# Optimization experiments

Hardware: AMD Instinct MI355X
Metric: run time of the kernel (lower is better)

Reference implementation:

```python
import jax, jax.numpy as jnp
import numpy as np

B, T, LC = 64, 256, 16          # batch, seq_len, max word (char) length
WV, CV = 50000, 128             # word / char vocab
CE, WE = 100, 300               # char / word embedding dims
CH, WH = 100, 300               # char lstm hidden, word lstm hidden per direction
NT = 20                         # num tags
PAD, START, STOP = 0, 18, 19
NEG = -10000.0


def lstm(x, mask, W_ih, W_hh, b_ih, b_hh, reverse=False):
    """Masked LSTM (packed-sequence semantics). x:(N,L,D), mask:(N,L).
    Returns outputs (N,L,H) zeroed at padded steps and the final carried hidden (N,H)."""
    N = x.shape[0]
    H = W_hh.shape[1]
    h0 = jnp.zeros((N, H), x.dtype)
    c0 = jnp.zeros((N, H), x.dtype)

    def step(carry, inp):
        h, c = carry
        xt, mt = inp  # (N,D), (N,1)
        g = xt @ W_ih.T + h @ W_hh.T + (b_ih + b_hh)
        i, f, gg, o = jnp.split(g, 4, axis=-1)  # torch gate order i,f,g,o
        i = jax.nn.sigmoid(i); f = jax.nn.sigmoid(f)
        gg = jnp.tanh(gg); o = jax.nn.sigmoid(o)
        c_new = f * c + i * gg
        h_new = o * jnp.tanh(c_new)
        h = mt * h_new + (1.0 - mt) * h
        c = mt * c_new + (1.0 - mt) * c
        return (h, c), h * mt

    (hT, _), outs = jax.lax.scan(step, (h0, c0),
                                 (x.transpose(1, 0, 2), mask.T[:, :, None]),
                                 reverse=reverse)
    return outs.transpose(1, 0, 2), hT


def setup_inputs() -> dict:
    key = jax.random.key(0)
    ks = jax.random.split(key, 16)
    # trailing-padded word sequences (pack_padded semantics)
    lengths = jax.random.randint(ks[0], (B,), T // 4, T + 1)
    wmask = jnp.arange(T)[None, :] < lengths[:, None]
    word_x = jnp.where(wmask, jax.random.randint(ks[1], (B, T), 1, WV), 0)
    clens = jax.random.randint(ks[2], (B * T,), 1, LC + 1)
    cmask = (jnp.arange(LC)[None, :] < clens[:, None]) & wmask.reshape(-1)[:, None]
    char_x = jnp.where(cmask, jax.random.randint(ks[3], (B * T, LC), 1, CV), 0)
    y = jnp.where(wmask, jax.random.randint(ks[4], (B, T), 1, START), 0)

    def xav(k, shape):
        return jax.random.uniform(k, shape, jnp.float32, -1.0, 1.0) * jnp.sqrt(6.0 / (shape[0] + shape[1]))

    tr = jax.random.normal(ks[14], (NT, NT), jnp.float32)
    tr = tr.at[START, :].set(NEG).at[:, STOP].set(NEG)
    tr = tr.at[:, PAD].set(NEG).at[PAD, :].set(NEG)
    tr = tr.at[PAD, STOP].set(0.0).at[PAD, PAD].set(0.0)

    return dict(
        word_x=word_x, char_x=char_x, y=y,
        word_emb=jax.random.normal(ks[5], (WV, WE), jnp.float32) * 0.1,
        char_emb=jax.random.normal(ks[6], (CV, CE), jnp.float32) * 0.1,
        cW_ih=xav(ks[7], (4 * CH, CE)), cW_hh=xav(ks[8], (4 * CH, CH)),
        cb_ih=jnp.zeros(4 * CH), cb_hh=jnp.zeros(4 * CH),
        fW_ih=xav(ks[9], (4 * WH, WE + CH)), fW_hh=xav(ks[10], (4 * WH, WH)),
        fb_ih=jnp.zeros(4 * WH), fb_hh=jnp.zeros(4 * WH),
        bW_ih=xav(ks[11], (4 * WH, WE + CH)), bW_hh=xav(ks[12], (4 * WH, WH)),
        bb_ih=jnp.zeros(4 * WH), bb_hh=jnp.zeros(4 * WH),
        out_W=xav(ks[13], (NT, 2 * WH)), out_b=jnp.zeros(NT),
        transition=tr,
    )


def _forward(word_x, char_x, y, word_emb, char_emb,
             cW_ih, cW_hh, cb_ih, cb_hh,
             fW_ih, fW_hh, fb_ih, fb_hh,
             bW_ih, bW_hh, bb_ih, bb_hh,
             out_W, out_b, transition):
    mask = (word_x > 0).astype(jnp.float32)          # (B,T)
    cmask = (char_x > 0).astype(jnp.float32)         # (B*T,LC)
    # char LSTM: final carried hidden == output at last valid char; 0 for empty words
    _, c_h = lstm(char_emb[char_x], cmask, cW_ih, cW_hh, cb_ih, cb_hh)
    feat = jnp.concatenate([word_emb[word_x], c_h.reshape(B, T, CH)], axis=-1)  # (B,T,400)
    f_out, _ = lstm(feat, mask, fW_ih, fW_hh, fb_ih, fb_hh)
    b_out, _ = lstm(feat, mask, bW_ih, bW_hh, bb_ih, bb_hh, reverse=True)
    h = jnp.concatenate([f_out, b_out], axis=-1) @ out_W.T + out_b  # (B,T,NT)
    h = h * mask[:, :, None]

    # CRF log-partition (forward recurrence)
    def step(alpha, inp):
        ht, mt = inp  # (B,NT), (B,1)
        a_t = jax.nn.logsumexp(alpha[:, None, :] + transition[None, :, :] + ht[:, :, None], axis=-1)
        return mt * a_t + (1.0 - mt) * alpha, None

    alpha0 = jnp.full((B, NT), NEG, jnp.float32).at[:, START].set(0.0)
    alpha, _ = jax.lax.scan(step, alpha0, (h.transpose(1, 0, 2), mask.T[:, :, None]))
    Z = jax.nn.logsumexp(alpha + transition[STOP], axis=-1)  # (B,)

    # gold path score
    y_ext = jnp.concatenate([jnp.full((B, 1), START, y.dtype), y], axis=1)  # (B,T+1)
    emis = jnp.take_along_axis(h, y[:, :, None], axis=2)[..., 0]            # (B,T)
    tr_t = transition[y_ext[:, 1:], y_ext[:, :-1]]                          # (B,T)
    score = ((emis + tr_t) * mask).sum(axis=1)
    lengths = mask.sum(axis=1).astype(jnp.int32)
    last = jnp.take_along_axis(y_ext, lengths[:, None], axis=1)[:, 0]
    score = score + transition[STOP, last]
    return Z - score  # (B,) per-sequence NLL


def reference(word_x, char_x, y, word_emb, char_emb,
              cW_ih, cW_hh, cb_ih, cb_hh,
              fW_ih, fW_hh, fb_ih, fb_hh,
              bW_ih, bW_hh, bb_ih, bb_hh,
              out_W, out_b, transition):
    return _forward(word_x, char_x, y, word_emb, char_emb,
                    cW_ih, cW_hh, cb_ih, cb_hh,
                    fW_ih, fW_hh, fb_ih, fb_hh,
                    bW_ih, bW_hh, bb_ih, bb_hh,
                    out_W, out_b, transition)
```

## Files before the change

### kernel.cpp

```cpp
#include <hip/hip_runtime.h>

#define B_ 64
#define T_ 256
#define LC_ 16
#define CV_ 128
#define CE_ 100
#define WE_ 300
#define CH_ 100
#define WH_ 300
#define NTAG 20
#define START_ 18
#define STOP_ 19
#define NEG_ -10000.0f
#define NSEQ (B_*T_)
#define GW (4*WH_)
#define KF (WE_+CH_)
#define NW_ 25
#define UH_ 12
#define ROW_DW 164
#define SLOT_DW (64*ROW_DW)
#define HH_DW (2*257*SLOT_DW)
#define ZBLK ((HH_DW + 64 + 255)/256)

typedef unsigned short ushort_t;
typedef __attribute__((ext_vector_type(8))) short bf16x8;
typedef __attribute__((ext_vector_type(4))) float f32x4;
union BF8 { bf16x8 v; ushort_t u[8]; };

__device__ inline float bf2f(ushort_t u){ return __uint_as_float(((unsigned int)u)<<16); }
__device__ inline ushort_t f2bf(float f){
  unsigned int x = __float_as_uint(f);
  unsigned int r = (x + 0x7fffu + ((x>>16)&1u)) >> 16;
  return (ushort_t)r;
}
__device__ inline float sigm(float x){ return 1.f/(1.f+__expf(-x)); }
__device__ inline float ftanh(float x){
  float ax = fabsf(x);
  float e = __expf(-2.f*ax);
  float t = (1.f-e)/(1.f+e);
  return copysignf(t, x);
}
__device__ inline void gload_lds16(const unsigned* g, unsigned* l){
  __builtin_amdgcn_global_load_lds((const __attribute__((address_space(1))) unsigned*)g,
                                   (__attribute__((address_space(3))) unsigned*)l, 16, 0, 17);
}

__global__ __launch_bounds__(256) void k_prep(unsigned int* __restrict__ hh, int* __restrict__ flags,
    const float* __restrict__ cemb, const float* __restrict__ cWih,
    const float* __restrict__ cbih, const float* __restrict__ cbhh, float* __restrict__ Ec_t){
  int bid = blockIdx.x;
  if (bid < ZBLK){
    size_t idx = (size_t)bid*256 + threadIdx.x;
    if (idx < HH_DW) hh[idx] = 0u;
    else if (idx < HH_DW + 64) flags[idx - HH_DW] = 0;
  } else {
    int idx = (bid - ZBLK)*256 + threadIdx.x;
    int r = idx >> 7, c = idx & 127;
    float a = cbih[r] + cbhh[r];
    for (int k=0;k<CE_;++k) a += cemb[c*CE_+k]*cWih[r*CE_+k];
    Ec_t[c*400 + r] = a;
  }
}

__global__ __launch_bounds__(256) void k_char(const float* __restrict__ Ec_t,
    const float* __restrict__ Whh, const int* __restrict__ char_x,
    ushort_t* __restrict__ c_h){
  extern __shared__ char csm[];
  ushort_t* h_lds = (ushort_t*)csm;
  float*    g_lds = (float*)(csm + 64*132*2);
  const int tid  = threadIdx.x;
  const int lane = tid & 63;
  const int w    = tid >> 6;
  const int tb   = w*6;
  bf16x8 Bf[7][4];
  {
    int ntile = (w==3) ? 7 : 6;
    for (int tt=0; tt<ntile; ++tt){
      int r = (tb+tt)*16 + (lane & 15);
      #pragma unroll
      for (int ks=0; ks<4; ++ks){
        BF8 tmp;
        #pragma unroll
        for (int j=0; j<8; ++j){
          int k = 32*ks + 8*(lane>>4) + j;
          tmp.u[j] = (k < CH_) ? f2bf(Whh[(size_t)r*CH_ + k]) : (ushort_t)0;
        }
        Bf[tt][ks] = tmp.v;
      }
    }
  }
  for (int i=tid; i<64*132; i+=256) h_lds[i] = 0;
  const int seq_l = tid & 63;
  const int us    = tid >> 6;
  const int seqg  = blockIdx.x*64 + seq_l;
  const int u0    = us*25;
  float c_r[25], h_r[25];
  #pragma unroll
  for (int j=0;j<25;++j){ c_r[j]=0.f; h_r[j]=0.f; }
  const int* cx = char_x + (size_t)seqg*LC_;
  __syncthreads();
  #pragma unroll 1
  for (int t=0; t<LC_; ++t){
    #pragma unroll
    for (int m=0; m<4; ++m){
      int abase = (16*m + (lane&15))*132 + 8*(lane>>4);
      bf16x8 a0 = *(const bf16x8*)(h_lds + abase);
      bf16x8 a1 = *(const bf16x8*)(h_lds + abase + 32);
      bf16x8 a2 = *(const bf16x8*)(h_lds + abase + 64);
      bf16x8 a3 = *(const bf16x8*)(h_lds + abase + 96);
      int rw = 16*m + 4*(lane>>4);
      #pragma unroll
      for (int tt=0; tt<6; ++tt){
        f32x4 acc = {0,0,0,0};
        acc = __builtin_amdgcn_mfma_f32_16x16x32_bf16(a0, Bf[tt][0], acc, 0,0,0);
        acc = __builtin_amdgcn_mfma_f32_16x16x32_bf16(a1, Bf[tt][1], acc, 0,0,0);
        acc = __builtin_amdgcn_mfma_f32_16x16x32_bf16(a2, Bf[tt][2], acc, 0,0,0);
        acc = __builtin_amdgcn_mfma_f32_16x16x32_bf16(a3, Bf[tt][3], acc, 0,0,0);
        int col = (tb+tt)*16 + (lane&15);
        #pragma unroll
        for (int r4=0;r4<4;++r4) g_lds[(rw+r4)*401 + col] = acc[r4];
      }
      if (w == 3){
        f32x4 acc = {0,0,0,0};
        acc = __builtin_amdgcn_mfma_f32_16x16x32_bf16(a0, Bf[6][0], acc, 0,0,0);
        acc = __builtin_amdgcn_mfma_f32_16x16x32_bf16(a1, Bf[6][1], acc, 0,0,0);
        acc = __builtin_amdgcn_mfma_f32_16x16x32_bf16(a2, Bf[6][2], acc, 0,0,0);
        acc = __builtin_amdgcn_mfma_f32_16x16x32_bf16(a3, Bf[6][3], acc, 0,0,0);
        int col = 24*16 + (lane&15);
        #pragma unroll
        for (int r4=0;r4<4;++r4) g_lds[(rw+r4)*401 + col] = acc[r4];
      }
    }
    int ch = cx[t];
    __syncthreads();
    {
      const float* ec = Ec_t + (size_t)ch*400;
      const float* gr = g_lds + seq_l*401;
      #pragma unroll
      for (int j=0;j<25;++j){
        int u = u0 + j;
        float gi = gr[u        ] + ec[u        ];
        float gf = gr[100 + u  ] + ec[100 + u  ];
        float gg = gr[200 + u  ] + ec[200 + u  ];
        float go = gr[300 + u  ] + ec[300 + u  ];
        float I = sigm(gi), F = sigm(gf), G = ftanh(gg), O = sigm(go);
        float cn = F*c_r[j] + I*G;
        float hn = O*ftanh(cn);
        if (ch > 0){ c_r[j] = cn; h_r[j] = hn; }
        h_lds[seq_l*132 + u] = f2bf(h_r[j]);
      }
    }
    __syncthreads();
  }
  #pragma unroll
  for (int j=0;j<25;++j) c_h[(size_t)seqg*CH_ + u0 + j] = f2bf(h_r[j]);
}

__global__ __launch_bounds__(256) void k_feat(const int* __restrict__ word_x,
    const float* __restrict__ wemb, const ushort_t* __restrict__ c_h,
    ushort_t* __restrict__ feat){
  int gid = blockIdx.x*256 + threadIdx.x;
  int rf = gid / 100;
  int j4 = gid - rf*100;
  int k = 4*j4;
  int t = rf >> 6, b = rf & 63;
  int seq = b*T_ + t;
  ushort4 u;
  if (k < WE_){
    int wid = word_x[seq];
    float4 v = *(const float4*)&wemb[(size_t)wid*WE_ + k];
    u.x=f2bf(v.x); u.y=f2bf(v.y); u.z=f2bf(v.z); u.w=f2bf(v.w);
  } else {
    u = *(const ushort4*)&c_h[(size_t)seq*CH_ + (k - WE_)];
  }
  *(ushort4*)&feat[(size_t)rf*KF + k] = u;
}

__global__ __launch_bounds__(512, 2) void k_word2(
    const ushort_t* __restrict__ feat, unsigned int* __restrict__ hhd,
    const float* __restrict__ fWih, const float* __restrict__ fWhh,
    const float* __restrict__ fbih, const float* __restrict__ fbhh,
    const float* __restrict__ bWih, const float* __restrict__ bWhh,
    const float* __restrict__ bbih, const float* __restrict__ bbhh,
    const int* __restrict__ word_x, int* __restrict__ flags){
  extern __shared__ char smem[];
  ushort_t* h_s    = (ushort_t*)smem;
  ushort_t* f_s    = (ushort_t*)(smem + 64*328*2);
  float*    g_s    = (float*)   (smem + 64*328*2 + 64*416*2);
  unsigned* mask_s = (unsigned*)(smem + 64*328*2 + 64*416*2 + 64*52*4);
  const int tid  = threadIdx.x;
  const int lane = tid & 63;
  const int w    = tid >> 6;
  const int dir  = blockIdx.x & 1;
  const int g    = blockIdx.x >> 1;
  const int u0   = g * UH_;
  const int tm   = w & 3;
  const int grp  = w >> 2;
  const bool two = (grp == 0);
  const int tnb  = grp ? 2 : 0;
  const float* Wih = dir ? bWih : fWih;
  const float* Whh = dir ? bWhh : fWhh;
  const float* bi  = dir ? bbih : fbih;
  const float* bh  = dir ? bbhh : fbhh;
  int* myflags = flags + dir*32;

  bf16x8 B2[2][13], B1[2][10];
  {
    const int kb = 8*(lane >> 4);
    #pragma unroll
    for (int ti=0; ti<2; ++ti){
      if (ti == 0 || two){
        int nl = 16*(tnb+ti) + (lane & 15);
        int r  = (nl & 3)*WH_ + u0 + (nl >> 2);
        #pragma unroll
        for (int kk=0; kk<13; ++kk){
          BF8 tmp;
          #pragma unroll
          for (int j=0; j<8; ++j){
            int k = 32*kk + kb + j;
            tmp.u[j] = (k < KF) ? f2bf(Wih[(size_t)r*KF + k]) : (ushort_t)0;
          }
          B2[ti][kk] = tmp.v;
        }
        #pragma unroll
        for (int kk=0; kk<10; ++kk){
          BF8 tmp;
          #pragma unroll
          for (int j=0; j<8; ++j){
            int k = 32*kk + kb + j;
            tmp.u[j] = (k < WH_) ? f2bf(Whh[(size_t)r*WH_ + k]) : (ushort_t)0;
          }
          B1[ti][kk] = tmp.v;
        }
      }
    }
  }
  for (int idx=tid; idx<64*16; idx+=512){ f_s[(idx>>4)*416 + 400 + (idx & 15)] = 0; }
  if (tid < 512){
    int row = tid >> 3, dw = tid & 7;
    const int* wp = word_x + row*T_ + dw*32;
    unsigned bits = 0u;
    #pragma unroll
    for (int j4=0; j4<8; ++j4){
      int4 v = *(const int4*)(wp + 4*j4);
      bits |= (v.x>0 ? 1u:0u) << (4*j4);
      bits |= (v.y>0 ? 1u:0u) << (4*j4+1);
      bits |= (v.z>0 ? 1u:0u) << (4*j4+2);
      bits |= (v.w>0 ? 1u:0u) << (4*j4+3);
    }
    mask_s[row*8 + dw] = bits;
  }

  const int m_u = tid & 63;
  const int up  = tid >> 6;
  float4 bias_a = {0,0,0,0}, bias_b = {0,0,0,0};
  if (tid < 384){
    int u = u0 + 2*up;
    bias_a.x = bi[0*WH_+u] + bh[0*WH_+u];
    bias_a.y = bi[1*WH_+u] + bh[1*WH_+u];
    bias_a.z = bi[2*WH_+u] + bh[2*WH_+u];
    bias_a.w = bi[3*WH_+u] + bh[3*WH_+u];
    bias_b.x = bi[0*WH_+u+1] + bh[0*WH_+u+1];
    bias_b.y = bi[1*WH_+u+1] + bh[1*WH_+u+1];
    bias_b.z = bi[2*WH_+u+1] + bh[2*WH_+u+1];
    bias_b.w = bi[3*WH_+u+1] + bh[3*WH_+u+1];
  }
  float c_a=0.f, h_a=0.f, c_b=0.f, h_b=0.f;
  const int arow_f = (16*tm + (lane&15))*416 + 8*(lane>>4);
  const int arow_h = (16*tm + (lane&15))*328 + 8*(lane>>4);
  unsigned* h_sd = (unsigned*)h_s;
  __syncthreads();

  #pragma unroll 1
  for (int s=0; s<T_; ++s){
    int t = dir ? (T_-1-s) : s;
    {
      const ushort_t* fsrc = feat + (size_t)t*64*KF;
      for (int idx=tid; idx<3200; idx+=512){
        int m = idx/50, j = idx - m*50;
        uint4 v = *(const uint4*)(fsrc + m*KF + 8*j);
        *(uint4*)(f_s + m*416 + 8*j) = v;
      }
    }
    if (w == 0 && s > 0){
      bool act = lane < NW_;
      for (int it=0; it<2000000; ++it){
        int f = act ? __hip_atomic_load(myflags + lane, __ATOMIC_RELAXED, __HIP_MEMORY_SCOPE_AGENT)
                    : 0x7fffffff;
        if (__all(f >= s)) break;
        __builtin_amdgcn_s_sleep(1);
      }
    }
    __syncthreads();
    {
      const unsigned* hsrc = hhd + (size_t)(dir*257 + s)*SLOT_DW;
      #pragma unroll
      for (int i=0;i<6;++i){
        int idx = tid + 512*i;
        if (i < 5 || idx < 2624) gload_lds16(hsrc + 4*idx, h_sd + 4*idx);
      }
    }
    f32x4 acc0a = {0,0,0,0}, acc0b = {0,0,0,0}, acc1a = {0,0,0,0}, acc1b = {0,0,0,0};
    #pragma unroll
    for (int kk=0; kk<13; ++kk){
      bf16x8 a = *(const bf16x8*)(f_s + arow_f + 32*kk);
      if (kk & 1){
        acc0b = __builtin_amdgcn_mfma_f32_16x16x32_bf16(a, B2[0][kk], acc0b, 0,0,0);
        if (two) acc1b = __builtin_amdgcn_mfma_f32_16x16x32_bf16(a, B2[1][kk], acc1b, 0,0,0);
      } else {
        acc0a = __builtin_amdgcn_mfma_f32_16x16x32_bf16(a, B2[0][kk], acc0a, 0,0,0);
        if (two) acc1a = __builtin_amdgcn_mfma_f32_16x16x32_bf16(a, B2[1][kk], acc1a, 0,0,0);
      }
    }
    asm volatile("s_waitcnt vmcnt(0)" ::: "memory");
    __syncthreads();
    #pragma unroll
    for (int kk=0; kk<10; ++kk){
      bf16x8 a = *(const bf16x8*)(h_s + arow_h + 32*kk);
      if (kk & 1){
        acc0b = __builtin_amdgcn_mfma_f32_16x16x32_bf16(a, B1[0][kk], acc0b, 0,0,0);
        if (two) acc1b = __builtin_amdgcn_mfma_f32_16x16x32_bf16(a, B1[1][kk], acc1b, 0,0,0);
      } else {
        acc0a = __builtin_amdgcn_mfma_f32_16x16x32_bf16(a, B1[0][kk], acc0a, 0,0,0);
        if (two) acc1a = __builtin_amdgcn_mfma_f32_16x16x32_bf16(a, B1[1][kk], acc1a, 0,0,0);
      }
    }
    {
      int nb = 16*tnb + (lane & 15);
      int mr = 16*tm + 4*(lane >> 4);
      f32x4 s0 = acc0a + acc0b;
      #pragma unroll
      for (int r4=0; r4<4; ++r4) g_s[(mr+r4)*52 + nb] = s0[r4];
      if (two){
        f32x4 s1 = acc1a + acc1b;
        #pragma unroll
        for (int r4=0; r4<4; ++r4) g_s[(mr+r4)*52 + nb + 16] = s1[r4];
      }
    }
    __syncthreads();
    if (tid < 384){
      int mt = (mask_s[m_u*8 + (t>>5)] >> (t&31)) & 1u;
      float4 ga = *(const float4*)(g_s + m_u*52 + 8*up);
      float4 gb = *(const float4*)(g_s + m_u*52 + 8*up + 4);
      {
        float gi = sigm (ga.x + bias_a.x);
        float gf = sigm (ga.y + bias_a.y);
        float gg = ftanh(ga.z + bias_a.z);
        float go = sigm (ga.w + bias_a.w);
        float cn = gf*c_a + gi*gg;
        float hn = go*ftanh(cn);
        if (mt){ c_a = cn; h_a = hn; }
      }
      {
        float gi = sigm (gb.x + bias_b.x);
        float gf = sigm (gb.y + bias_b.y);
        float gg = ftanh(gb.z + bias_b.z);
        float go = sigm (gb.w + bias_b.w);
        float cn = gf*c_b + gi*gg;
        float hn = go*ftanh(cn);
        if (mt){ c_b = cn; h_b = hn; }
      }
      unsigned pack = (unsigned)f2bf(h_a) | ((unsigned)f2bf(h_b) << 16);
      unsigned* hdst = hhd + (size_t)(dir*257 + s + 1)*SLOT_DW + m_u*ROW_DW + g*6 + up;
      __hip_atomic_store(hdst, pack, __ATOMIC_RELAXED, __HIP_MEMORY_SCOPE_AGENT);
    }
    asm volatile("s_waitcnt vmcnt(0)" ::: "memory");
    __syncthreads();
    if (tid == 0)
      __hip_atomic_store(myflags + g, s + 1, __ATOMIC_RELAXED, __HIP_MEMORY_SCOPE_AGENT);
  }
}

__global__ __launch_bounds__(320) void k_logits(const unsigned int* __restrict__ hhd,
    const float* __restrict__ outW, const float* __restrict__ outb, float* __restrict__ lg){
  extern __shared__ char lsm[];
  float*    w_l = (float*)lsm;
  ushort_t* h_l = (ushort_t*)(lsm + 20*608*4);
  int tid = threadIdx.x;
  for (int idx=tid; idx<20*608; idx+=320){
    int tag = idx/608, k = idx - tag*608;
    w_l[idx] = (k < 600) ? outW[(size_t)tag*600 + k] : 0.f;
  }
  unsigned* hld = (unsigned*)h_l;
  int seq0 = blockIdx.x*16;
  for (int idx=tid; idx<16*304; idx+=320){
    int m = idx/304, d = idx - m*304;
    unsigned v = 0u;
    if (d < 300){
      int dir = d >= 150;
      int dd = d - dir*150;
      int seq = seq0 + m;
      int b = seq >> 8, t = seq & 255;
      int slot = dir ? (T_ - t) : (t + 1);
      v = hhd[(size_t)(dir*257 + slot)*SLOT_DW + b*ROW_DW + dd];
    }
    hld[m*304 + d] = v;
  }
  __syncthreads();
  int sq = tid/20, tag = tid - sq*20;
  const ushort_t* hr = h_l + sq*608;
  const float*    wr = w_l + tag*608;
  float acc = 0.f;
  #pragma unroll
  for (int jj=0; jj<152; ++jj){
    ushort4 h4 = *(const ushort4*)(hr + 4*jj);
    float4  wv = *(const float4*)(wr + 4*jj);
    acc += bf2f(h4.x)*wv.x + bf2f(h4.y)*wv.y + bf2f(h4.z)*wv.z + bf2f(h4.w)*wv.w;
  }
  lg[(size_t)(seq0+sq)*NTAG + tag] = acc + outb[tag];
}

__global__ __launch_bounds__(64) void k_crf(const float* __restrict__ lg,
    const float* __restrict__ tr, const int* __restrict__ word_x,
    const int* __restrict__ y, float* __restrict__ out){
  int b = blockIdx.x, lane = threadIdx.x;
  float trr[20];
  if (lane < NTAG){
    #pragma unroll
    for (int j=0;j<NTAG;++j) trr[j] = tr[lane*NTAG + j];
  }
  float tstop = (lane < NTAG) ? tr[STOP_*NTAG + lane] : NEG_;
  unsigned mbits = 0u;
  if (lane < 8){
    const int* wp = word_x + b*T_ + lane*32;
    #pragma unroll
    for (int j4=0; j4<8; ++j4){
      int4 v = *(const int4*)(wp + 4*j4);
      mbits |= (v.x>0 ? 1u:0u) << (4*j4);
      mbits |= (v.y>0 ? 1u:0u) << (4*j4+1);
      mbits |= (v.z>0 ? 1u:0u) << (4*j4+2);
      mbits |= (v.w>0 ? 1u:0u) << (4*j4+3);
    }
  }
  const float* lgb = lg + (size_t)b*T_*NTAG;
  float alpha = (lane == START_) ? 0.f : NEG_;
  float hv_cur = lgb[lane];
  #pragma unroll 1
  for (int t=0; t<T_; ++t){
    float hv_next = (t < T_-1) ? lgb[(size_t)(t+1)*NTAG + lane] : 0.f;
    unsigned mrow = __shfl(mbits, t >> 5);
    int mt = (mrow >> (t & 31)) & 1;
    float aj[20];
    #pragma unroll
    for (int j=0;j<NTAG;++j) aj[j] = __shfl(alpha, j) + trr[j];
    float mx = -3.4e38f;
    #pragma unroll
    for (int j=0;j<NTAG;++j) mx = fmaxf(mx, aj[j]);
    float ss = 0.f;
    #pragma unroll
    for (int j=0;j<NTAG;++j) ss += __expf(aj[j] - mx);
    float anew = __logf(ss) + mx + hv_cur;
    if (mt && lane < NTAG) alpha = anew;
    hv_cur = hv_next;
  }
  float val = alpha + tstop;
  float mx = -3.4e38f;
  #pragma unroll
  for (int j=0;j<NTAG;++j) mx = fmaxf(mx, __shfl(val, j));
  float ss = 0.f;
  #pragma unroll
  for (int j=0;j<NTAG;++j) ss += __expf(__shfl(val, j) - mx);
  float Z = __logf(ss) + mx;
  float sc = 0.f; int cnt = 0;
  #pragma unroll 1
  for (int qq=0;qq<4;++qq){
    int t = lane + 64*qq;
    if (word_x[b*T_ + t] > 0){
      int yt = y[b*T_ + t];
      int yp = (t == 0) ? START_ : y[b*T_ + t - 1];
      sc += lgb[(size_t)t*NTAG + yt] + tr[yt*NTAG + yp];
      cnt++;
    }
  }
  for (int off=32; off; off>>=1){
    sc += __shfl_down(sc, off);
    cnt += __shfl_down(cnt, off);
  }
  if (lane == 0){
    int last = y[b*T_ + cnt - 1];
    sc += tr[STOP_*NTAG + last];
    out[b] = Z - sc;
  }
}

extern "C" void kernel_launch(void* const* d_in, const int* in_sizes, int n_in,
                              void* d_out, int out_size, void* d_ws, size_t ws_size,
                              hipStream_t stream) {
  (void)in_sizes; (void)n_in; (void)out_size; (void)ws_size;
  const int*   word_x  = (const int*)  d_in[0];
  const int*   char_x  = (const int*)  d_in[1];
  const int*   y       = (const int*)  d_in[2];
  const float* wemb    = (const float*)d_in[3];
  const float* cemb    = (const float*)d_in[4];
  const float* cWih    = (const float*)d_in[5];
  const float* cWhh    = (const float*)d_in[6];
  const float* cbih    = (const float*)d_in[7];
  const float* cbhh    = (const float*)d_in[8];
  const float* fWih    = (const float*)d_in[9];
  const float* fWhh    = (const float*)d_in[10];
  const float* fbih    = (const float*)d_in[11];
  const float* fbhh    = (const float*)d_in[12];
  const float* bWih    = (const float*)d_in[13];
  const float* bWhh    = (const float*)d_in[14];
  const float* bbih    = (const float*)d_in[15];
  const float* bbhh    = (const float*)d_in[16];
  const float* outW    = (const float*)d_in[17];
  const float* outb    = (const float*)d_in[18];
  const float* trans   = (const float*)d_in[19];
  float* out = (float*)d_out;

  char* ws = (char*)d_ws;
  float*        Ec_t   = (float*)       (ws + 0);
  ushort_t*     c_h    = (ushort_t*)    (ws + 204800);
  ushort_t*     feat   = (ushort_t*)    (ws + 3481600);
  unsigned int* hh     = (unsigned int*)(ws + 16588800);
  int*          flags  = (int*)         (ws + 38168576);
  float*        lg     = (float*)       (ws + 38168832);

  static const int LDS_W = 64*328*2 + 64*416*2 + 64*52*4 + 64*8*4;
  static const int LDS_C = 64*132*2 + 64*401*4;
  static const int LDS_L = 20*608*4 + 16*608*2;
  hipFuncSetAttribute((const void*)k_word2, hipFuncAttributeMaxDynamicSharedMemorySize, LDS_W);
  hipFuncSetAttribute((const void*)k_char,  hipFuncAttributeMaxDynamicSharedMemorySize, LDS_C);
  hipFuncSetAttribute((const void*)k_logits,hipFuncAttributeMaxDynamicSharedMemorySize, LDS_L);

  hipLaunchKernelGGL(k_prep, dim3(ZBLK + 200), dim3(256), 0, stream, hh, flags, cemb, cWih, cbih, cbhh, Ec_t);
  hipLaunchKernelGGL(k_char, dim3(256), dim3(256), LDS_C, stream, Ec_t, cWhh, char_x, c_h);
  hipLaunchKernelGGL(k_feat, dim3(6400), dim3(256), 0, stream, word_x, wemb, c_h, feat);
  hipLaunchKernelGGL(k_word2, dim3(2*NW_), dim3(512), LDS_W, stream,
                     feat, hh, fWih, fWhh, fbih, fbhh, bWih, bWhh, bbih, bbhh, word_x, flags);
  hipLaunchKernelGGL(k_logits, dim3(NSEQ/16), dim3(320), LDS_L, stream, hh, outW, outb, lg);
  hipLaunchKernelGGL(k_crf, dim3(64), dim3(64), 0, stream, lg, trans, word_x, y, out);
}
```

Before: 1.969 ms.

## Double-buffer word features in LDS via async loads and write char states into feat

The word LSTM kernel no longer copies each timestep's feature tile from global to LDS with synchronous loads. It now prefetches the next step's tile into an alternate LDS buffer using global_load_lds, overlapping that transfer with the recurrent MFMA work, and reuses the current feature buffer as gate scratch. The feat layout is padded to 416 columns so the async copy is contiguous. The char LSTM now writes its hidden states directly into the padded feat buffer, which removes the separate c_h intermediate and its extra pass. The cost is more LDS per block, which may affect occupancy, plus a tighter coupling between the gate scratch and the feature buffer.

Measured after the change: 1.751 ms. -11.1%, faster.

```diff
diff --git a/kernel.cpp b/kernel.cpp
--- a/kernel.cpp
+++ b/kernel.cpp
@@ -13,8 +13,7 @@
 #define STOP_ 19
 #define NEG_ -10000.0f
 #define NSEQ (B_*T_)
-#define GW (4*WH_)
-#define KF (WE_+CH_)
+#define KFP 416
 #define NW_ 25
 #define UH_ 12
 #define ROW_DW 164
@@ -40,9 +39,13 @@
   float t = (1.f-e)/(1.f+e);
   return copysignf(t, x);
 }
-__device__ inline void gload_lds16(const unsigned* g, unsigned* l){
+__device__ inline void gload16_byp(const unsigned* g, unsigned* l){
   __builtin_amdgcn_global_load_lds((const __attribute__((address_space(1))) unsigned*)g,
                                    (__attribute__((address_space(3))) unsigned*)l, 16, 0, 17);
+}
+__device__ inline void gload16(const unsigned* g, unsigned* l){
+  __builtin_amdgcn_global_load_lds((const __attribute__((address_space(1))) unsigned*)g,
+                                   (__attribute__((address_space(3))) unsigned*)l, 16, 0, 0);
 }
 
 __global__ __launch_bounds__(256) void k_prep(unsigned int* __restrict__ hh, int* __restrict__ flags,
@@ -64,7 +67,7 @@
 
 __global__ __launch_bounds__(256) void k_char(const float* __restrict__ Ec_t,
     const float* __restrict__ Whh, const int* __restrict__ char_x,
-    ushort_t* __restrict__ c_h){
+    ushort_t* __restrict__ feat){
   extern __shared__ char csm[];
   ushort_t* h_lds = (ushort_t*)csm;
   float*    g_lds = (float*)(csm + 64*132*2);
@@ -152,28 +155,29 @@
     }
     __syncthreads();
   }
-  #pragma unroll
-  for (int j=0;j<25;++j) c_h[(size_t)seqg*CH_ + u0 + j] = f2bf(h_r[j]);
+  {
+    int bb = seqg >> 8, tt2 = seqg & 255;
+    ushort_t* dst = feat + (size_t)(tt2*64 + bb)*KFP + WE_ + u0;
+    #pragma unroll
+    for (int j=0;j<25;++j) dst[j] = f2bf(h_r[j]);
+  }
 }
 
 __global__ __launch_bounds__(256) void k_feat(const int* __restrict__ word_x,
-    const float* __restrict__ wemb, const ushort_t* __restrict__ c_h,
-    ushort_t* __restrict__ feat){
+    const float* __restrict__ wemb, ushort_t* __restrict__ feat){
   int gid = blockIdx.x*256 + threadIdx.x;
-  int rf = gid / 100;
-  int j4 = gid - rf*100;
+  int rf = gid / 104;
+  int j4 = gid - rf*104;
   int k = 4*j4;
   int t = rf >> 6, b = rf & 63;
-  int seq = b*T_ + t;
-  ushort4 u;
+  ushort4 u = make_ushort4(0,0,0,0);
   if (k < WE_){
+    int seq = b*T_ + t;
     int wid = word_x[seq];
     float4 v = *(const float4*)&wemb[(size_t)wid*WE_ + k];
     u.x=f2bf(v.x); u.y=f2bf(v.y); u.z=f2bf(v.z); u.w=f2bf(v.w);
-  } else {
-    u = *(const ushort4*)&c_h[(size_t)seq*CH_ + (k - WE_)];
-  }
-  *(ushort4*)&feat[(size_t)rf*KF + k] = u;
+  }
+  *(ushort4*)&feat[(size_t)rf*KFP + k] = u;
 }
 
 __global__ __launch_bounds__(512, 2) void k_word2(
@@ -185,9 +189,9 @@
     const int* __restrict__ word_x, int* __restrict__ flags){
   extern __shared__ char smem[];
   ushort_t* h_s    = (ushort_t*)smem;
-  ushort_t* f_s    = (ushort_t*)(smem + 64*328*2);
-  float*    g_s    = (float*)   (smem + 64*328*2 + 64*416*2);
-  unsigned* mask_s = (unsigned*)(smem + 64*328*2 + 64*416*2 + 64*52*4);
+  ushort_t* f_sb0  = (ushort_t*)(smem + 41984);
+  ushort_t* f_sb1  = (ushort_t*)(smem + 41984 + 53248);
+  unsigned* mask_s = (unsigned*)(smem + 41984 + 106496);
   const int tid  = threadIdx.x;
   const int lane = tid & 63;
   const int w    = tid >> 6;
@@ -218,7 +222,7 @@
           #pragma unroll
           for (int j=0; j<8; ++j){
             int k = 32*kk + kb + j;
-            tmp.u[j] = (k < KF) ? f2bf(Wih[(size_t)r*KF + k]) : (ushort_t)0;
+            tmp.u[j] = (k < 400) ? f2bf(Wih[(size_t)r*400 + k]) : (ushort_t)0;
           }
           B2[ti][kk] = tmp.v;
         }
@@ -235,7 +239,6 @@
       }
     }
   }
-  for (int idx=tid; idx<64*16; idx+=512){ f_s[(idx>>4)*416 + 400 + (idx & 15)] = 0; }
   if (tid < 512){
     int row = tid >> 3, dw = tid & 7;
     const int* wp = word_x + row*T_ + dw*32;
@@ -266,22 +269,28 @@
     bias_b.w = bi[3*WH_+u+1] + bh[3*WH_+u+1];
   }
   float c_a=0.f, h_a=0.f, c_b=0.f, h_b=0.f;
-  const int arow_f = (16*tm + (lane&15))*416 + 8*(lane>>4);
+  const int arow_f = (16*tm + (lane&15))*KFP + 8*(lane>>4);
   const int arow_h = (16*tm + (lane&15))*328 + 8*(lane>>4);
   unsigned* h_sd = (unsigned*)h_s;
+
+  {
+    int t0 = dir ? (T_-1) : 0;
+    const unsigned* fsrc = (const unsigned*)(feat + (size_t)t0*64*KFP);
+    unsigned* fdl = (unsigned*)f_sb0;
+    #pragma unroll
+    for (int i=0;i<7;++i){
+      int idx = tid + 512*i;
+      if (i < 6 || idx < 3328) gload16(fsrc + 4*idx, fdl + 4*idx);
+    }
+  }
+  asm volatile("s_waitcnt vmcnt(0)" ::: "memory");
   __syncthreads();
 
   #pragma unroll 1
   for (int s=0; s<T_; ++s){
     int t = dir ? (T_-1-s) : s;
-    {
-      const ushort_t* fsrc = feat + (size_t)t*64*KF;
-      for (int idx=tid; idx<3200; idx+=512){
-        int m = idx/50, j = idx - m*50;
-        uint4 v = *(const uint4*)(fsrc + m*KF + 8*j);
-        *(uint4*)(f_s + m*416 + 8*j) = v;
-      }
-    }
+    const ushort_t* f_cur = (s & 1) ? f_sb1 : f_sb0;
+    float* g_s = (float*)f_cur;
     if (w == 0 && s > 0){
       bool act = lane < NW_;
       for (int it=0; it<2000000; ++it){
@@ -297,13 +306,13 @@
       #pragma unroll
       for (int i=0;i<6;++i){
         int idx = tid + 512*i;
-        if (i < 5 || idx < 2624) gload_lds16(hsrc + 4*idx, h_sd + 4*idx);
+        if (i < 5 || idx < 2624) gload16_byp(hsrc + 4*idx, h_sd + 4*idx);
       }
     }
     f32x4 acc0a = {0,0,0,0}, acc0b = {0,0,0,0}, acc1a = {0,0,0,0}, acc1b = {0,0,0,0};
     #pragma unroll
     for (int kk=0; kk<13; ++kk){
-      bf16x8 a = *(const bf16x8*)(f_s + arow_f + 32*kk);
+      bf16x8 a = *(const bf16x8*)(f_cur + arow_f + 32*kk);
       if (kk & 1){
         acc0b = __builtin_amdgcn_mfma_f32_16x16x32_bf16(a, B2[0][kk], acc0b, 0,0,0);
         if (two) acc1b = __builtin_amdgcn_mfma_f32_16x16x32_bf16(a, B2[1][kk], acc1b, 0,0,0);
@@ -314,6 +323,16 @@
     }
     asm volatile("s_waitcnt vmcnt(0)" ::: "memory");
     __syncthreads();
+    if (s + 1 < T_){
+      int tn = dir ? (T_-2-s) : (s+1);
+      const unsigned* fsrc = (const unsigned*)(feat + (size_t)tn*64*KFP);
+      unsigned* fdl = (unsigned*)((s & 1) ? f_sb0 : f_sb1);
+      #pragma unroll
+      for (int i=0;i<7;++i){
+        int idx = tid + 512*i;
+        if (i < 6 || idx < 3328) gload16(fsrc + 4*idx, fdl + 4*idx);
+      }
+    }
     #pragma unroll
     for (int kk=0; kk<10; ++kk){
       bf16x8 a = *(const bf16x8*)(h_s + arow_h + 32*kk);
@@ -511,13 +530,12 @@
 
   char* ws = (char*)d_ws;
   float*        Ec_t   = (float*)       (ws + 0);
-  ushort_t*     c_h    = (ushort_t*)    (ws + 204800);
-  ushort_t*     feat   = (ushort_t*)    (ws + 3481600);
-  unsigned int* hh     = (unsigned int*)(ws + 16588800);
-  int*          flags  = (int*)         (ws + 38168576);
-  float*        lg     = (float*)       (ws + 38168832);
-
-  static const int LDS_W = 64*328*2 + 64*416*2 + 64*52*4 + 64*8*4;
+  ushort_t*     feat   = (ushort_t*)    (ws + 204800);
+  unsigned int* hh     = (unsigned int*)(ws + 13836288);
+  int*          flags  = (int*)         (ws + 35416064);
+  float*        lg     = (float*)       (ws + 35416320);
+
+  static const int LDS_W = 41984 + 2*53248 + 2048;
   static const int LDS_C = 64*132*2 + 64*401*4;
   static const int LDS_L = 20*608*4 + 16*608*2;
   hipFuncSetAttribute((const void*)k_word2, hipFuncAttributeMaxDynamicSharedMemorySize, LDS_W);
@@ -525,8 +543,8 @@
   hipFuncSetAttribute((const void*)k_logits,hipFuncAttributeMaxDynamicSharedMemorySize, LDS_L);
 
   hipLaunchKernelGGL(k_prep, dim3(ZBLK + 200), dim3(256), 0, stream, hh, flags, cemb, cWih, cbih, cbhh, Ec_t);
-  hipLaunchKernelGGL(k_char, dim3(256), dim3(256), LDS_C, stream, Ec_t, cWhh, char_x, c_h);
-  hipLaunchKernelGGL(k_feat, dim3(6400), dim3(256), 0, stream, word_x, wemb, c_h, feat);
+  hipLaunchKernelGGL(k_feat, dim3(6656), dim3(256), 0, stream, word_x, wemb, feat);
+  hipLaunchKernelGGL(k_char, dim3(256), dim3(256), LDS_C, stream, Ec_t, cWhh, char_x, feat);
   hipLaunchKernelGGL(k_word2, dim3(2*NW_), dim3(512), LDS_W, stream,
                      feat, hh, fWih, fWhh, fbih, fbhh, bWih, bWhh, bbih, bbhh, word_x, flags);
   hipLaunchKernelGGL(k_logits, dim3(NSEQ/16), dim3(320), LDS_L, stream, hh, outW, outb, lg);
```
